# Kernel tuning notes

Measured on AMD Instinct MI355X. Metric: run time of the kernel, lower is better.

## Reference

```python
import jax, jax.numpy as jnp
import numpy as np

N = 20000      # num nodes
E = 320000     # num edges (avg degree 16)
T = 12         # timesteps
IN = 128       # in_channels
GH = 64        # gnn_hidden_dim
RH = 128       # rnn_hidden_dim
OUT = 1        # out_channels


def setup_inputs() -> dict:
    key = jax.random.key(0)
    ks = jax.random.split(key, 8)
    x_seq = jax.random.normal(ks[0], (T, N, IN), jnp.float32)
    edge_index = jax.random.randint(ks[1], (2, E), 0, N, jnp.int32)
    init = lambda k, shape, fan: jax.random.normal(k, shape, jnp.float32) / np.sqrt(fan).astype(np.float32)
    gcn_w = init(ks[2], (IN, GH), IN)
    gcn_b = jnp.zeros((GH,), jnp.float32)
    w_ih = init(ks[3], (4 * RH, GH), GH)   # torch LSTM gate order: i, f, g, o
    w_hh = init(ks[4], (4 * RH, RH), RH)
    b_ih = jnp.zeros((4 * RH,), jnp.float32)
    b_hh = jnp.zeros((4 * RH,), jnp.float32)
    fc_w = init(ks[5], (OUT, RH), RH)
    fc_b = jnp.zeros((OUT,), jnp.float32)
    return {"x_seq": x_seq, "edge_index": edge_index, "gcn_w": gcn_w, "gcn_b": gcn_b,
            "w_ih": w_ih, "w_hh": w_hh, "b_ih": b_ih, "b_hh": b_hh,
            "fc_w": fc_w, "fc_b": fc_b}


def _gcn_norm(edge_index, n_nodes, dtype):
    # Add self loops, then symmetric normalization D^{-1/2} (A+I) D^{-1/2}.
    loop = jnp.arange(n_nodes, dtype=edge_index.dtype)
    src = jnp.concatenate([edge_index[0], loop])
    dst = jnp.concatenate([edge_index[1], loop])
    deg = jax.ops.segment_sum(jnp.ones(src.shape[0], dtype), dst, num_segments=n_nodes)
    dinv = jnp.where(deg > 0, jax.lax.rsqrt(deg), jnp.zeros((), dtype))
    norm = dinv[src] * dinv[dst]  # [E+N]
    return src, dst, norm


def reference(x_seq, edge_index, gcn_w, gcn_b, w_ih, w_hh, b_ih, b_hh, fc_w, fc_b):
    n_nodes = x_seq.shape[1]
    src, dst, norm = _gcn_norm(edge_index, n_nodes, x_seq.dtype)

    def gcn_step(_, x):  # x: [N, IN]
        h = x @ gcn_w                                  # [N, GH] transform first (GH < IN)
        msg = h[src] * norm[:, None]                   # gather + normalize: [E+N, GH]
        out = jax.ops.segment_sum(msg, dst, num_segments=n_nodes) + gcn_b
        return None, out

    _, hs = jax.lax.scan(gcn_step, None, x_seq)        # [T, N, GH]

    bias = b_ih + b_hh

    def lstm_step(carry, x):  # x: [N, GH]
        h, c = carry
        gates = x @ w_ih.T + h @ w_hh.T + bias         # [N, 4*RH]
        i, f, g, o = jnp.split(gates, 4, axis=-1)
        i = jax.nn.sigmoid(i)
        f = jax.nn.sigmoid(f)
        g = jnp.tanh(g)
        o = jax.nn.sigmoid(o)
        c = f * c + i * g
        h = o * jnp.tanh(c)
        return (h, c), None

    h0 = jnp.zeros((n_nodes, w_hh.shape[1]), x_seq.dtype)
    (h_last, _), _ = jax.lax.scan(lstm_step, (h0, h0), hs)
    return h_last @ fc_w.T + fc_b                      # [N, OUT]
```

## Files before the change

### kernel.cpp

```cpp
#include <hip/hip_runtime.h>

constexpr int NN = 20000;
constexpr int NE = 320000;
constexpr int TT = 12;
constexpr int CIN = 128;
constexpr int GH = 64;
constexpr int RH = 128;
constexpr int TOTAL = TT * NN;

typedef __attribute__((ext_vector_type(8))) short short8;
typedef __attribute__((ext_vector_type(4))) float f32x4;

__device__ __forceinline__ float rcp_fast(float x) { return __builtin_amdgcn_rcpf(x); }
__device__ __forceinline__ float sigf(float x) { return rcp_fast(1.0f + __expf(-x)); }
__device__ __forceinline__ float tanh_fast(float x) { return 1.0f - 2.0f * rcp_fast(__expf(2.0f * x) + 1.0f); }

__device__ __forceinline__ unsigned short f2b_rn(float x) {
    union { float f; unsigned int u; } v; v.f = x;
    unsigned int r = v.u + 0x7FFFu + ((v.u >> 16) & 1u);
    return (unsigned short)(r >> 16);
}
__device__ __forceinline__ float b2f_lo(unsigned int u) {
    union { unsigned int u; float f; } v; v.u = u << 16;
    return v.f;
}
__device__ __forceinline__ float b2f_hi(unsigned int u) {
    union { unsigned int u; float f; } v; v.u = u & 0xFFFF0000u;
    return v.f;
}

__device__ __forceinline__ void gload_lds16(const void* g, void* l) {
    __builtin_amdgcn_global_load_lds((const __attribute__((address_space(1))) void*)g,
                                     (__attribute__((address_space(3))) void*)l, 16, 0, 0);
}


__global__ __launch_bounds__(256) void degree_kernel(const int* __restrict__ dst, int* __restrict__ deg) {
    int e = blockIdx.x * blockDim.x + threadIdx.x;
    if (e < NE) atomicAdd(&deg[dst[e]], 1);
}

__global__ __launch_bounds__(1024) void scan_kernel(const int* __restrict__ deg, int* __restrict__ row_ptr,
                                                    int* __restrict__ cursor, float* __restrict__ dinv) {
    __shared__ int sums[1024];
    int t = threadIdx.x;
    const int per = (NN + 1023) / 1024;
    int start = t * per;
    int end = min(start + per, NN);
    int s = 0;
    for (int i = start; i < end; ++i) s += deg[i];
    sums[t] = s;
    __syncthreads();
    for (int off = 1; off < 1024; off <<= 1) {
        int v = (t >= off) ? sums[t - off] : 0;
        __syncthreads();
        sums[t] += v;
        __syncthreads();
    }
    int run = (t == 0) ? 0 : sums[t - 1];
    for (int i = start; i < end; ++i) {
        row_ptr[i] = run;
        cursor[i] = run;
        run += deg[i];
        dinv[i] = rsqrtf((float)deg[i] + 1.0f);
    }
    if (t == 1023) row_ptr[NN] = sums[1023];
}

__global__ __launch_bounds__(256) void scatter_kernel(const int* __restrict__ src, const int* __restrict__ dst,
                                                      const float* __restrict__ dinv, int* __restrict__ cursor,
                                                      int* __restrict__ csr_src, float* __restrict__ csr_norm) {
    int e = blockIdx.x * blockDim.x + threadIdx.x;
    if (e >= NE) return;
    int d = dst[e], s = src[e];
    int pos = atomicAdd(&cursor[d], 1);
    csr_src[pos] = s;
    csr_norm[pos] = dinv[s] * dinv[d];
}


__global__ __launch_bounds__(256) void wprep_all_kernel(const float* __restrict__ w_ih, const float* __restrict__ w_hh,
                                                        const float* __restrict__ gcn_w,
                                                        const float* __restrict__ b_ih, const float* __restrict__ b_hh,
                                                        unsigned short* __restrict__ wp, unsigned short* __restrict__ wx,
                                                        float* __restrict__ bias) {
    int i = blockIdx.x * blockDim.x + threadIdx.x;
    if (i < 12288) {
        int gs = i & 3;
        int col = (i >> 2) & 511;
        int chunk = i >> 11;
        int g = gs ^ ((col >> 1) & 3);
        int k0 = chunk * 32 + g * 8;
        short8 v;
#pragma unroll
        for (int j = 0; j < 8; ++j) {
            int k = k0 + j;
            float f = (k < 64) ? w_ih[col * 64 + k] : w_hh[col * 128 + (k - 64)];
            v[j] = (short)f2b_rn(f);
        }
        *reinterpret_cast<short8*>(wp + (size_t)i * 8) = v;
    } else if (i < 13312) {
        int q = i - 12288;
        int gs = q & 3;
        int col = (q >> 2) & 63;
        int chunk = q >> 8;
        int g = gs ^ ((col >> 1) & 3);
        int k0 = chunk * 32 + g * 8;
        short8 v;
#pragma unroll
        for (int j = 0; j < 8; ++j) v[j] = (short)f2b_rn(gcn_w[(k0 + j) * 64 + col]);
        *reinterpret_cast<short8*>(wx + (size_t)q * 8) = v;
    } else if (i < 13824) {
        int q = i - 13312;
        bias[q] = b_ih[q] + b_hh[q];
    }
}


__global__ __launch_bounds__(256) void xw_mfma_kernel(const float* __restrict__ x,
                                                      const unsigned short* __restrict__ wx,
                                                      unsigned short* __restrict__ xwb) {
    __shared__ __align__(16) char As[4 * 4096];
    __shared__ __align__(16) char Bs[4 * 4096];
    int tid = threadIdx.x;
    int lane = tid & 63, w = tid >> 6;
    int m0 = blockIdx.x * 64;

#pragma unroll
    for (int j = 0; j < 4; ++j) {
        const unsigned short* src = wx + (size_t)(w * 4 + j) * 512 + lane * 8;
        gload_lds16(src, Bs + (w * 4 + j) * 1024);
    }
    {
        int row = tid >> 2, gs = tid & 3;
        int srow = m0 + row;
        int g = gs ^ ((row >> 1) & 3);
        const float* sp = x + (size_t)srow * CIN + g * 8;
#pragma unroll
        for (int c = 0; c < 4; ++c) {
            float4 f0 = *reinterpret_cast<const float4*>(sp + c * 32);
            float4 f1 = *reinterpret_cast<const float4*>(sp + c * 32 + 4);
            short8 v;
            v[0] = (short)f2b_rn(f0.x); v[1] = (short)f2b_rn(f0.y);
            v[2] = (short)f2b_rn(f0.z); v[3] = (short)f2b_rn(f0.w);
            v[4] = (short)f2b_rn(f1.x); v[5] = (short)f2b_rn(f1.y);
            v[6] = (short)f2b_rn(f1.z); v[7] = (short)f2b_rn(f1.w);
            *reinterpret_cast<short8*>(As + c * 4096 + row * 64 + gs * 16) = v;
        }
    }
    __syncthreads();

    f32x4 acc[4] = {};
    int rl = w * 16 + (lane & 15);
    int o = lane >> 4;
#pragma unroll
    for (int c = 0; c < 4; ++c) {
        int gsa = o ^ ((rl >> 1) & 3);
        short8 a = *reinterpret_cast<const short8*>(As + c * 4096 + rl * 64 + gsa * 16);
#pragma unroll
        for (int cn = 0; cn < 4; ++cn) {
            int col = cn * 16 + (lane & 15);
            int gsb = o ^ ((col >> 1) & 3);
            short8 b = *reinterpret_cast<const short8*>(Bs + c * 4096 + col * 64 + gsb * 16);
            acc[cn] = __builtin_amdgcn_mfma_f32_16x16x32_bf16(a, b, acc[cn], 0, 0, 0);
        }
    }
#pragma unroll
    for (int cn = 0; cn < 4; ++cn)
#pragma unroll
        for (int r = 0; r < 4; ++r) {
            int row = m0 + w * 16 + (lane >> 4) * 4 + r;
            int col = cn * 16 + (lane & 15);
            xwb[(size_t)row * GH + col] = f2b_rn(acc[cn][r]);
        }
}


__global__ __launch_bounds__(256) void gather_kernel(const unsigned short* __restrict__ xwb, const float* __restrict__ dinv,
                                                     const int* __restrict__ row_ptr, const int* __restrict__ csr_src,
                                                     const float* __restrict__ csr_norm, const float* __restrict__ gcn_b,
                                                     unsigned short* __restrict__ hs_b) {
    int t0 = blockIdx.y * 2;
    int wpair = (blockIdx.x * blockDim.x + threadIdx.x) >> 6;
    int lane = threadIdx.x & 63;
    int g = lane >> 5, sl = lane & 31;
    int node = wpair * 2 + g;
    const unsigned int* sl0 = (const unsigned int*)(xwb + (size_t)t0 * NN * GH);
    const unsigned int* sl1 = sl0 + (size_t)NN * 32;

    float dv = dinv[node];
    float b0 = gcn_b[sl * 2], b1 = gcn_b[sl * 2 + 1];
    unsigned int u0 = sl0[(size_t)node * 32 + sl];
    unsigned int u1 = sl1[(size_t)node * 32 + sl];
    float a0x = b0 + dv * dv * b2f_lo(u0);
    float a0y = b1 + dv * dv * b2f_hi(u0);
    float a1x = b0 + dv * dv * b2f_lo(u1);
    float a1y = b1 + dv * dv * b2f_hi(u1);

    int e0 = row_ptr[node];
    int deg = row_ptr[node + 1] - e0;
    int degA = __shfl(deg, 0), degB = __shfl(deg, 32);
    int dmax = max(degA, degB);

    for (int base = 0; base < dmax; base += 32) {
        int cnt = min(deg - base, 32);
        bool valid = sl < cnt;
        int myidx = valid ? csr_src[e0 + base + sl] : 0;
        float mynm = valid ? csr_norm[e0 + base + sl] : 0.f;
        int c8 = (max(cnt, 0) + 7) & ~7;
        int c8o = __shfl(c8, (1 - g) << 5);
        int c8w = max(c8, c8o);
        for (int j = 0; j < c8w; j += 8) {
            int s0 = __shfl(myidx, (g << 5) + j + 0), s1 = __shfl(myidx, (g << 5) + j + 1);
            int s2 = __shfl(myidx, (g << 5) + j + 2), s3 = __shfl(myidx, (g << 5) + j + 3);
            int s4 = __shfl(myidx, (g << 5) + j + 4), s5 = __shfl(myidx, (g << 5) + j + 5);
            int s6 = __shfl(myidx, (g << 5) + j + 6), s7 = __shfl(myidx, (g << 5) + j + 7);
            float n0 = __shfl(mynm, (g << 5) + j + 0), n1 = __shfl(mynm, (g << 5) + j + 1);
            float n2 = __shfl(mynm, (g << 5) + j + 2), n3 = __shfl(mynm, (g << 5) + j + 3);
            float n4 = __shfl(mynm, (g << 5) + j + 4), n5 = __shfl(mynm, (g << 5) + j + 5);
            float n6 = __shfl(mynm, (g << 5) + j + 6), n7 = __shfl(mynm, (g << 5) + j + 7);
            unsigned int p0 = sl0[(size_t)s0 * 32 + sl], q0 = sl1[(size_t)s0 * 32 + sl];
            unsigned int p1 = sl0[(size_t)s1 * 32 + sl], q1 = sl1[(size_t)s1 * 32 + sl];
            unsigned int p2 = sl0[(size_t)s2 * 32 + sl], q2 = sl1[(size_t)s2 * 32 + sl];
            unsigned int p3 = sl0[(size_t)s3 * 32 + sl], q3 = sl1[(size_t)s3 * 32 + sl];
            unsigned int p4 = sl0[(size_t)s4 * 32 + sl], q4 = sl1[(size_t)s4 * 32 + sl];
            unsigned int p5 = sl0[(size_t)s5 * 32 + sl], q5 = sl1[(size_t)s5 * 32 + sl];
            unsigned int p6 = sl0[(size_t)s6 * 32 + sl], q6 = sl1[(size_t)s6 * 32 + sl];
            unsigned int p7 = sl0[(size_t)s7 * 32 + sl], q7 = sl1[(size_t)s7 * 32 + sl];
            a0x += n0 * b2f_lo(p0); a0y += n0 * b2f_hi(p0); a1x += n0 * b2f_lo(q0); a1y += n0 * b2f_hi(q0);
            a0x += n1 * b2f_lo(p1); a0y += n1 * b2f_hi(p1); a1x += n1 * b2f_lo(q1); a1y += n1 * b2f_hi(q1);
            a0x += n2 * b2f_lo(p2); a0y += n2 * b2f_hi(p2); a1x += n2 * b2f_lo(q2); a1y += n2 * b2f_hi(q2);
            a0x += n3 * b2f_lo(p3); a0y += n3 * b2f_hi(p3); a1x += n3 * b2f_lo(q3); a1y += n3 * b2f_hi(q3);
            a0x += n4 * b2f_lo(p4); a0y += n4 * b2f_hi(p4); a1x += n4 * b2f_lo(q4); a1y += n4 * b2f_hi(q4);
            a0x += n5 * b2f_lo(p5); a0y += n5 * b2f_hi(p5); a1x += n5 * b2f_lo(q5); a1y += n5 * b2f_hi(q5);
            a0x += n6 * b2f_lo(p6); a0y += n6 * b2f_hi(p6); a1x += n6 * b2f_lo(q6); a1y += n6 * b2f_hi(q6);
            a0x += n7 * b2f_lo(p7); a0y += n7 * b2f_hi(p7); a1x += n7 * b2f_lo(q7); a1y += n7 * b2f_hi(q7);
        }
    }
    unsigned int o0 = (unsigned int)f2b_rn(a0x) | ((unsigned int)f2b_rn(a0y) << 16);
    unsigned int o1 = (unsigned int)f2b_rn(a1x) | ((unsigned int)f2b_rn(a1y) << 16);
    ((unsigned int*)hs_b)[((size_t)t0 * NN + node) * 32 + sl] = o0;
    ((unsigned int*)hs_b)[((size_t)(t0 + 1) * NN + node) * 32 + sl] = o1;
}


#define HS_OFF 0
#define HA_OFF 20480
#define RED_OFF 61440
#define SMEM_BYTES 64000

__global__ __launch_bounds__(512, 2) void lstm_persist_kernel(const unsigned short* __restrict__ hs_all,
                                                              const unsigned short* __restrict__ wp,
                                                              const float* __restrict__ bias,
                                                              const float* __restrict__ fc_w,
                                                              const float* __restrict__ fc_b,
                                                              float* __restrict__ out) {
    __shared__ __align__(16) char smem[SMEM_BYTES];
    int tid = threadIdx.x;
    int lane = tid & 63, w = tid >> 6;
    int l15 = lane & 15, o = lane >> 4;
    int base = blockIdx.x * 80;

    int sw = o ^ ((l15 >> 1) & 3);
    int colbase = w * 16 + l15;
    float bi = bias[colbase], bff = bias[128 + colbase], bg = bias[256 + colbase], bo = bias[384 + colbase];
    float fcw = fc_w[colbase];
    f32x4 binit[4] = {{bi, bi, bi, bi}, {bff, bff, bff, bff}, {bg, bg, bg, bg}, {bo, bo, bo, bo}};

    int h_chunk = w >> 1;
    int h_g = ((w & 1) << 1) + (l15 >> 3);
    int h_j = l15 & 7;

    short8 breg[6][4];
#pragma unroll
    for (int c = 0; c < 6; ++c)
#pragma unroll
        for (int g = 0; g < 4; ++g) {
            size_t goff = ((size_t)(c * 512 + g * 128 + colbase) * 4 + sw) * 8;
            breg[c][g] = *reinterpret_cast<const short8*>(wp + goff);
            asm volatile("" : "+v"(breg[c][g]));
        }

    {
#pragma unroll
        for (int i = 0; i < 10; ++i) ((int*)(smem + HA_OFF))[tid + i * 512] = 0;
#pragma unroll
        for (int j = 0; j < 2; ++j) {
            int gi = j * 512 + tid;
            if (gi < 640) {
                int cc = (gi >= 320) ? 1 : 0;
                int rem = gi - cc * 320;
                int row = rem >> 2, gs = rem & 3;
                int g = gs ^ ((row >> 1) & 3);
                const unsigned short* src = hs_all + ((size_t)(base + row)) * 64 + cc * 32 + g * 8;
                gload_lds16(src, smem + HS_OFF + gi * 16);
            }
        }
    }
    __syncthreads();

    float c_reg[5][4] = {};
    f32x4 acc[5][4];

#pragma unroll 1
    for (int t = 0; t < TT; ++t) {
        if (t + 1 < TT) {
            char* dstb = smem + HS_OFF + ((t + 1) & 1) * 10240;
#pragma unroll
            for (int j = 0; j < 2; ++j) {
                int gi = j * 512 + tid;
                if (gi < 640) {
                    int cc = (gi >= 320) ? 1 : 0;
                    int rem = gi - cc * 320;
                    int row = rem >> 2, gs = rem & 3;
                    int g = gs ^ ((row >> 1) & 3);
                    const unsigned short* src = hs_all + ((size_t)(t + 1) * NN + base + row) * 64 + cc * 32 + g * 8;
                    gload_lds16(src, dstb + gi * 16);
                }
            }
        }

#pragma unroll
        for (int mi = 0; mi < 5; ++mi)
#pragma unroll
            for (int g = 0; g < 4; ++g) acc[mi][g] = binit[g];

        const char* hsb = smem + HS_OFF + (t & 1) * 10240;
        const char* hab = smem + HA_OFF + (t & 1) * 20480;
        __builtin_amdgcn_s_setprio(1);
#pragma unroll
        for (int c = 0; c < 6; ++c) {
            const char* abase = (c < 2) ? (hsb + c * 5120) : (hab + (c - 2) * 5120);
            short8 a[5];
#pragma unroll
            for (int mi = 0; mi < 5; ++mi)
                a[mi] = *reinterpret_cast<const short8*>(abase + (mi * 16 + l15) * 64 + sw * 16);
#pragma unroll
            for (int g = 0; g < 4; ++g)
#pragma unroll
                for (int mi = 0; mi < 5; ++mi)
                    acc[mi][g] = __builtin_amdgcn_mfma_f32_16x16x32_bf16(a[mi], breg[c][g], acc[mi][g], 0, 0, 0);
        }
        __builtin_amdgcn_s_setprio(0);

        char* hwr = smem + HA_OFF + ((t + 1) & 1) * 20480;
        if (t + 1 < TT) {
#pragma unroll
            for (int mi = 0; mi < 5; ++mi)
#pragma unroll
                for (int r = 0; r < 4; ++r) {
                    float iv = sigf(acc[mi][0][r]);
                    float fv = sigf(acc[mi][1][r]);
                    float gv = tanh_fast(acc[mi][2][r]);
                    float ov = sigf(acc[mi][3][r]);
                    float cnew = fv * c_reg[mi][r] + iv * gv;
                    c_reg[mi][r] = cnew;
                    float hv = ov * tanh_fast(cnew);
                    int row = mi * 16 + o * 4 + r;
                    int gs_h = h_g ^ ((row >> 1) & 3);
                    *(unsigned short*)(hwr + h_chunk * 5120 + row * 64 + gs_h * 16 + h_j * 2) = f2b_rn(hv);
                }
        } else {
#pragma unroll
            for (int mi = 0; mi < 5; ++mi)
#pragma unroll
                for (int r = 0; r < 4; ++r) {
                    float iv = sigf(acc[mi][0][r]);
                    float fv = sigf(acc[mi][1][r]);
                    float gv = tanh_fast(acc[mi][2][r]);
                    float ov = sigf(acc[mi][3][r]);
                    float cnew = fv * c_reg[mi][r] + iv * gv;
                    float hv = ov * tanh_fast(cnew);
                    float p = hv * fcw;
                    p += __shfl_xor(p, 1);
                    p += __shfl_xor(p, 2);
                    p += __shfl_xor(p, 4);
                    p += __shfl_xor(p, 8);
                    if (l15 == 0) {
                        int row = mi * 16 + o * 4 + r;
                        ((float*)(smem + RED_OFF))[w * 80 + row] = p;
                    }
                }
        }
        __syncthreads();
    }

    if (tid < 80) {
        const float* red = (const float*)(smem + RED_OFF);
        float s = 0.f;
#pragma unroll
        for (int w8 = 0; w8 < 8; ++w8) s += red[w8 * 80 + tid];
        out[base + tid] = s + fc_b[0];
    }
}


extern "C" void kernel_launch(void* const* d_in, const int* in_sizes, int n_in,
                              void* d_out, int out_size, void* d_ws, size_t ws_size,
                              hipStream_t stream) {
    const float* x_seq = (const float*)d_in[0];
    const int* edge = (const int*)d_in[1];
    const float* gcn_w = (const float*)d_in[2];
    const float* gcn_b = (const float*)d_in[3];
    const float* w_ih = (const float*)d_in[4];
    const float* w_hh = (const float*)d_in[5];
    const float* b_ih = (const float*)d_in[6];
    const float* b_hh = (const float*)d_in[7];
    const float* fc_w = (const float*)d_in[8];
    const float* fc_b = (const float*)d_in[9];
    float* out = (float*)d_out;

    char* w = (char*)d_ws;
    auto carve = [&](size_t bytes) {
        void* p = (void*)w;
        w += (bytes + 255) & ~(size_t)255;
        return p;
    };
    float* dinv = (float*)carve(NN * 4);
    int* deg = (int*)carve(NN * 4);
    int* row_ptr = (int*)carve((NN + 1) * 4);
    int* cursor = (int*)carve(NN * 4);
    int* csr_src = (int*)carve(NE * 4);
    float* csr_norm = (float*)carve(NE * 4);
    unsigned short* xwb = (unsigned short*)carve((size_t)TOTAL * GH * 2);
    unsigned short* hs_b = (unsigned short*)carve((size_t)TOTAL * GH * 2);
    unsigned short* wp = (unsigned short*)carve((size_t)6 * 512 * 4 * 8 * 2);
    unsigned short* wx = (unsigned short*)carve((size_t)4 * 64 * 4 * 8 * 2);
    float* bias = (float*)carve(512 * 4);

    hipMemsetAsync(deg, 0, NN * 4, stream);

    const int* e_src = edge;
    const int* e_dst = edge + NE;

    degree_kernel<<<(NE + 255) / 256, 256, 0, stream>>>(e_dst, deg);
    scan_kernel<<<1, 1024, 0, stream>>>(deg, row_ptr, cursor, dinv);
    scatter_kernel<<<(NE + 255) / 256, 256, 0, stream>>>(e_src, e_dst, dinv, cursor, csr_src, csr_norm);
    wprep_all_kernel<<<54, 256, 0, stream>>>(w_ih, w_hh, gcn_w, b_ih, b_hh, wp, wx, bias);

    xw_mfma_kernel<<<TOTAL / 64, 256, 0, stream>>>(x_seq, wx, xwb);
    dim3 ggrid(NN / 2 / 4, TT / 2);
    gather_kernel<<<ggrid, 256, 0, stream>>>(xwb, dinv, row_ptr, csr_src, csr_norm, gcn_b, hs_b);
    lstm_persist_kernel<<<NN / 80, 512, 0, stream>>>(hs_b, wp, bias, fc_w, fc_b, out);
}
```

Before: 236.5 us.

## Store XW node-major across timesteps so gather reads all twelve steps per neighbor

```diff
diff --git a/kernel.cpp b/kernel.cpp
--- a/kernel.cpp
+++ b/kernel.cpp
@@ -119,12 +119,13 @@
 
 __global__ __launch_bounds__(256) void xw_mfma_kernel(const float* __restrict__ x,
                                                       const unsigned short* __restrict__ wx,
-                                                      unsigned short* __restrict__ xwb) {
+                                                      unsigned short* __restrict__ xwt) {
     __shared__ __align__(16) char As[4 * 4096];
     __shared__ __align__(16) char Bs[4 * 4096];
     int tid = threadIdx.x;
     int lane = tid & 63, w = tid >> 6;
-    int m0 = blockIdx.x * 64;
+    int t = blockIdx.y;
+    int n0 = blockIdx.x * 64;
 
 #pragma unroll
     for (int j = 0; j < 4; ++j) {
@@ -133,9 +134,9 @@
     }
     {
         int row = tid >> 2, gs = tid & 3;
-        int srow = m0 + row;
+        int node = min(n0 + row, NN - 1);
         int g = gs ^ ((row >> 1) & 3);
-        const float* sp = x + (size_t)srow * CIN + g * 8;
+        const float* sp = x + ((size_t)t * NN + node) * CIN + g * 8;
 #pragma unroll
         for (int c = 0; c < 4; ++c) {
             float4 f0 = *reinterpret_cast<const float4*>(sp + c * 32);
@@ -151,7 +152,8 @@
     __syncthreads();
 
     f32x4 acc[4] = {};
-    int rl = w * 16 + (lane & 15);
+    int l15 = lane & 15;
+    int rl = w * 16 + l15;
     int o = lane >> 4;
 #pragma unroll
     for (int c = 0; c < 4; ++c) {
@@ -159,7 +161,7 @@
         short8 a = *reinterpret_cast<const short8*>(As + c * 4096 + rl * 64 + gsa * 16);
 #pragma unroll
         for (int cn = 0; cn < 4; ++cn) {
-            int col = cn * 16 + (lane & 15);
+            int col = cn * 16 + l15;
             int gsb = o ^ ((col >> 1) & 3);
             short8 b = *reinterpret_cast<const short8*>(Bs + c * 4096 + col * 64 + gsb * 16);
             acc[cn] = __builtin_amdgcn_mfma_f32_16x16x32_bf16(a, b, acc[cn], 0, 0, 0);
@@ -169,78 +171,73 @@
     for (int cn = 0; cn < 4; ++cn)
 #pragma unroll
         for (int r = 0; r < 4; ++r) {
-            int row = m0 + w * 16 + (lane >> 4) * 4 + r;
-            int col = cn * 16 + (lane & 15);
-            xwb[(size_t)row * GH + col] = f2b_rn(acc[cn][r]);
-        }
-}
-
-
-__global__ __launch_bounds__(256) void gather_kernel(const unsigned short* __restrict__ xwb, const float* __restrict__ dinv,
+            int node = n0 + w * 16 + o * 4 + r;
+            int col = cn * 16 + l15;
+            if (node < NN) xwt[((size_t)node * TT + t) * 64 + col] = f2b_rn(acc[cn][r]);
+        }
+}
+
+
+__global__ __launch_bounds__(256) void gather_kernel(const unsigned short* __restrict__ xwt, const float* __restrict__ dinv,
                                                      const int* __restrict__ row_ptr, const int* __restrict__ csr_src,
                                                      const float* __restrict__ csr_norm, const float* __restrict__ gcn_b,
                                                      unsigned short* __restrict__ hs_b) {
-    int t0 = blockIdx.y * 2;
-    int wpair = (blockIdx.x * blockDim.x + threadIdx.x) >> 6;
+    int node = (blockIdx.x * blockDim.x + threadIdx.x) >> 6;
     int lane = threadIdx.x & 63;
     int g = lane >> 5, sl = lane & 31;
-    int node = wpair * 2 + g;
-    const unsigned int* sl0 = (const unsigned int*)(xwb + (size_t)t0 * NN * GH);
-    const unsigned int* sl1 = sl0 + (size_t)NN * 32;
+    if (node >= NN) return;
+    const unsigned int* xw32 = (const unsigned int*)xwt;
+    unsigned int mylane = g * 192 + sl;
 
     float dv = dinv[node];
+    float dd = dv * dv;
     float b0 = gcn_b[sl * 2], b1 = gcn_b[sl * 2 + 1];
-    unsigned int u0 = sl0[(size_t)node * 32 + sl];
-    unsigned int u1 = sl1[(size_t)node * 32 + sl];
-    float a0x = b0 + dv * dv * b2f_lo(u0);
-    float a0y = b1 + dv * dv * b2f_hi(u0);
-    float a1x = b0 + dv * dv * b2f_lo(u1);
-    float a1y = b1 + dv * dv * b2f_hi(u1);
+    float ax[6], ay[6];
+    {
+        unsigned int voff = (unsigned int)node * 384 + mylane;
+#pragma unroll
+        for (int k = 0; k < 6; ++k) {
+            unsigned int u = xw32[voff + k * 32];
+            ax[k] = b0 + dd * b2f_lo(u);
+            ay[k] = b1 + dd * b2f_hi(u);
+        }
+    }
 
     int e0 = row_ptr[node];
     int deg = row_ptr[node + 1] - e0;
-    int degA = __shfl(deg, 0), degB = __shfl(deg, 32);
-    int dmax = max(degA, degB);
-
-    for (int base = 0; base < dmax; base += 32) {
-        int cnt = min(deg - base, 32);
-        bool valid = sl < cnt;
-        int myidx = valid ? csr_src[e0 + base + sl] : 0;
-        float mynm = valid ? csr_norm[e0 + base + sl] : 0.f;
-        int c8 = (max(cnt, 0) + 7) & ~7;
-        int c8o = __shfl(c8, (1 - g) << 5);
-        int c8w = max(c8, c8o);
-        for (int j = 0; j < c8w; j += 8) {
-            int s0 = __shfl(myidx, (g << 5) + j + 0), s1 = __shfl(myidx, (g << 5) + j + 1);
-            int s2 = __shfl(myidx, (g << 5) + j + 2), s3 = __shfl(myidx, (g << 5) + j + 3);
-            int s4 = __shfl(myidx, (g << 5) + j + 4), s5 = __shfl(myidx, (g << 5) + j + 5);
-            int s6 = __shfl(myidx, (g << 5) + j + 6), s7 = __shfl(myidx, (g << 5) + j + 7);
-            float n0 = __shfl(mynm, (g << 5) + j + 0), n1 = __shfl(mynm, (g << 5) + j + 1);
-            float n2 = __shfl(mynm, (g << 5) + j + 2), n3 = __shfl(mynm, (g << 5) + j + 3);
-            float n4 = __shfl(mynm, (g << 5) + j + 4), n5 = __shfl(mynm, (g << 5) + j + 5);
-            float n6 = __shfl(mynm, (g << 5) + j + 6), n7 = __shfl(mynm, (g << 5) + j + 7);
-            unsigned int p0 = sl0[(size_t)s0 * 32 + sl], q0 = sl1[(size_t)s0 * 32 + sl];
-            unsigned int p1 = sl0[(size_t)s1 * 32 + sl], q1 = sl1[(size_t)s1 * 32 + sl];
-            unsigned int p2 = sl0[(size_t)s2 * 32 + sl], q2 = sl1[(size_t)s2 * 32 + sl];
-            unsigned int p3 = sl0[(size_t)s3 * 32 + sl], q3 = sl1[(size_t)s3 * 32 + sl];
-            unsigned int p4 = sl0[(size_t)s4 * 32 + sl], q4 = sl1[(size_t)s4 * 32 + sl];
-            unsigned int p5 = sl0[(size_t)s5 * 32 + sl], q5 = sl1[(size_t)s5 * 32 + sl];
-            unsigned int p6 = sl0[(size_t)s6 * 32 + sl], q6 = sl1[(size_t)s6 * 32 + sl];
-            unsigned int p7 = sl0[(size_t)s7 * 32 + sl], q7 = sl1[(size_t)s7 * 32 + sl];
-            a0x += n0 * b2f_lo(p0); a0y += n0 * b2f_hi(p0); a1x += n0 * b2f_lo(q0); a1y += n0 * b2f_hi(q0);
-            a0x += n1 * b2f_lo(p1); a0y += n1 * b2f_hi(p1); a1x += n1 * b2f_lo(q1); a1y += n1 * b2f_hi(q1);
-            a0x += n2 * b2f_lo(p2); a0y += n2 * b2f_hi(p2); a1x += n2 * b2f_lo(q2); a1y += n2 * b2f_hi(q2);
-            a0x += n3 * b2f_lo(p3); a0y += n3 * b2f_hi(p3); a1x += n3 * b2f_lo(q3); a1y += n3 * b2f_hi(q3);
-            a0x += n4 * b2f_lo(p4); a0y += n4 * b2f_hi(p4); a1x += n4 * b2f_lo(q4); a1y += n4 * b2f_hi(q4);
-            a0x += n5 * b2f_lo(p5); a0y += n5 * b2f_hi(p5); a1x += n5 * b2f_lo(q5); a1y += n5 * b2f_hi(q5);
-            a0x += n6 * b2f_lo(p6); a0y += n6 * b2f_hi(p6); a1x += n6 * b2f_lo(q6); a1y += n6 * b2f_hi(q6);
-            a0x += n7 * b2f_lo(p7); a0y += n7 * b2f_hi(p7); a1x += n7 * b2f_lo(q7); a1y += n7 * b2f_hi(q7);
-        }
-    }
-    unsigned int o0 = (unsigned int)f2b_rn(a0x) | ((unsigned int)f2b_rn(a0y) << 16);
-    unsigned int o1 = (unsigned int)f2b_rn(a1x) | ((unsigned int)f2b_rn(a1y) << 16);
-    ((unsigned int*)hs_b)[((size_t)t0 * NN + node) * 32 + sl] = o0;
-    ((unsigned int*)hs_b)[((size_t)(t0 + 1) * NN + node) * 32 + sl] = o1;
+    for (int base = 0; base < deg; base += 64) {
+        int cnt = min(deg - base, 64);
+        bool valid = lane < cnt;
+        int myidx = valid ? csr_src[e0 + base + lane] : 0;
+        float mynm = valid ? csr_norm[e0 + base + lane] : 0.f;
+        int c8 = (cnt + 7) & ~7;
+        for (int j = 0; j < c8; j += 8) {
+#pragma unroll
+            for (int jj = 0; jj < 8; ++jj) {
+                int si = __shfl(myidx, j + jj);
+                float ni = __shfl(mynm, j + jj);
+                unsigned int voff = (unsigned int)si * 384 + mylane;
+                unsigned int u0 = xw32[voff];
+                unsigned int u1 = xw32[voff + 32];
+                unsigned int u2 = xw32[voff + 64];
+                unsigned int u3 = xw32[voff + 96];
+                unsigned int u4 = xw32[voff + 128];
+                unsigned int u5 = xw32[voff + 160];
+                ax[0] += ni * b2f_lo(u0); ay[0] += ni * b2f_hi(u0);
+                ax[1] += ni * b2f_lo(u1); ay[1] += ni * b2f_hi(u1);
+                ax[2] += ni * b2f_lo(u2); ay[2] += ni * b2f_hi(u2);
+                ax[3] += ni * b2f_lo(u3); ay[3] += ni * b2f_hi(u3);
+                ax[4] += ni * b2f_lo(u4); ay[4] += ni * b2f_hi(u4);
+                ax[5] += ni * b2f_lo(u5); ay[5] += ni * b2f_hi(u5);
+            }
+        }
+    }
+
+    unsigned int* ob = (unsigned int*)hs_b;
+#pragma unroll
+    for (int k = 0; k < 6; ++k)
+        ob[((size_t)(g * 6 + k) * NN + node) * 32 + sl] =
+            (unsigned int)f2b_rn(ax[k]) | ((unsigned int)f2b_rn(ay[k]) << 16);
 }
 
 
@@ -422,7 +419,7 @@
     int* cursor = (int*)carve(NN * 4);
     int* csr_src = (int*)carve(NE * 4);
     float* csr_norm = (float*)carve(NE * 4);
-    unsigned short* xwb = (unsigned short*)carve((size_t)TOTAL * GH * 2);
+    unsigned short* xwt = (unsigned short*)carve((size_t)NN * TT * GH * 2);
     unsigned short* hs_b = (unsigned short*)carve((size_t)TOTAL * GH * 2);
     unsigned short* wp = (unsigned short*)carve((size_t)6 * 512 * 4 * 8 * 2);
     unsigned short* wx = (unsigned short*)carve((size_t)4 * 64 * 4 * 8 * 2);
@@ -438,8 +435,8 @@
     scatter_kernel<<<(NE + 255) / 256, 256, 0, stream>>>(e_src, e_dst, dinv, cursor, csr_src, csr_norm);
     wprep_all_kernel<<<54, 256, 0, stream>>>(w_ih, w_hh, gcn_w, b_ih, b_hh, wp, wx, bias);
 
-    xw_mfma_kernel<<<TOTAL / 64, 256, 0, stream>>>(x_seq, wx, xwb);
-    dim3 ggrid(NN / 2 / 4, TT / 2);
-    gather_kernel<<<ggrid, 256, 0, stream>>>(xwb, dinv, row_ptr, csr_src, csr_norm, gcn_b, hs_b);
+    dim3 xgrid((NN + 63) / 64, TT);
+    xw_mfma_kernel<<<xgrid, 256, 0, stream>>>(x_seq, wx, xwt);
+    gather_kernel<<<NN / 4, 256, 0, stream>>>(xwt, dinv, row_ptr, csr_src, csr_norm, gcn_b, hs_b);
     lstm_persist_kernel<<<NN / 80, 512, 0, stream>>>(hs_b, wp, bias, fc_w, fc_b, out);
 }
```

Result: slower. 263.4 us (+11.4%).
